# Performance work log

Measured on AMD Instinct MI355X. Metric: run time of the kernel, lower is better.

The kernel has to match this reference:

```python
import jax, jax.numpy as jnp
import numpy as np

H_DIM_EXP = 25  # n = 2**25 = 33,554,432

def setup_inputs() -> dict:
    key = jax.random.key(0)
    x = jax.random.normal(key, (2 ** H_DIM_EXP,), dtype=jnp.float32)
    return {"x": x, "h_dim_exp": H_DIM_EXP}

def reference(x, h_dim_exp):
    # Fast Walsh-Hadamard transform. The original views x as [1,2,2,...,2,1]
    # and applies a (+,-) butterfly along each of the log2(n) axes-of-size-2.
    # Butterfly stages on distinct bits commute, so we process bits from low
    # to high with rank-3 reshapes instead of a rank-(exp+2) tensor.
    y = x
    for i in range(h_dim_exp):
        y = y.reshape(-1, 2, 2 ** i)        # (n/2^{i+1}, 2, 2^i)
        a, b = y[:, 0, :], y[:, 1, :]
        y = jnp.stack([a + b, a - b], axis=1)
    return y.reshape(x.shape)
```

## Files before the change

kernel.cpp:

```cpp
#include <hip/hip_runtime.h>


__device__ __forceinline__ void bfly(float4& a, float4& b) {
  float ax = a.x, ay = a.y, az = a.z, aw = a.w;
  a.x = ax + b.x; a.y = ay + b.y; a.z = az + b.z; a.w = aw + b.w;
  b.x = ax - b.x; b.y = ay - b.y; b.z = az - b.z; b.w = aw - b.w;
}

__device__ __forceinline__ void cross4(float4 (&v)[16]) {
#pragma unroll
  for (int m = 0; m < 4; ++m) {
#pragma unroll
    for (int k = 0; k < 16; ++k) {
      if (!(k & (1 << m))) bfly(v[k], v[k | (1 << m)]);
    }
  }
}

__global__ __launch_bounds__(256) void wht_pass1(const float4* __restrict__ in4,
                                                 float4* __restrict__ out4) {
  __shared__ float4 lds[4096];
  const int t = threadIdx.x;
  const int base4 = (int)blockIdx.x << 12;
  float4 v[16];
#pragma unroll
  for (int k = 0; k < 16; ++k) v[k] = in4[base4 + t + (k << 8)];
#pragma unroll
  for (int k = 0; k < 16; ++k) {
    float4 a = v[k];
    float s0 = a.x + a.y, d0 = a.x - a.y, s1 = a.z + a.w, d1 = a.z - a.w;
    v[k].x = s0 + s1; v[k].y = d0 + d1; v[k].z = s0 - s1; v[k].w = d0 - d1;
  }
  cross4(v);

#pragma unroll
  for (int k = 0; k < 16; ++k) { int q = t + (k << 8); lds[q ^ ((q >> 4) & 15)] = v[k]; }
  __syncthreads();
#pragma unroll
  for (int u = 0; u < 16; ++u) { int q = u + (t << 4); v[u] = lds[q ^ ((q >> 4) & 15)]; }
  cross4(v);

#pragma unroll
  for (int u = 0; u < 16; ++u) { int q = u + (t << 4); lds[q ^ ((q >> 4) & 15)] = v[u]; }
  __syncthreads();
  const int c0 = t & 15, c1 = t >> 4;
#pragma unroll
  for (int u = 0; u < 16; ++u) {
    int q = c0 + (u << 4) + (c1 << 8);
    v[u] = lds[q ^ ((q >> 4) & 15)];
  }
  cross4(v);

#pragma unroll
  for (int u = 0; u < 16; ++u) out4[base4 + c0 + (u << 4) + (c1 << 8)] = v[u];
}

__global__ __launch_bounds__(1024, 4) void wht_pass2(float4* __restrict__ b4) {
  __shared__ float4 lds[4096];
  const int t = threadIdx.x;
  const int cb4 = (int)blockIdx.x << 3;
  const int c4 = t & 7;
  const int cc = t & 1;
  const int qt = (t >> 1) & 3;
  const int rlo = t >> 3;
  float4 v[16];
#pragma unroll
  for (int k = 0; k < 16; ++k)
    v[k] = b4[((long)(rlo + (k << 7)) << 12) + cb4 + c4];
  cross4(v);

#pragma unroll 1
  for (int r4 = 0; r4 < 4; ++r4) {
    __syncthreads();
    if (qt == r4) {
#pragma unroll
      for (int k = 0; k < 16; ++k) {
        int q = ((rlo + (k << 7)) << 1) | cc;
        lds[q ^ (((q >> 8) & 3) << 1)] = v[k];
      }
    }
    __syncthreads();
    if (qt == r4) {
#pragma unroll
      for (int rb = 0; rb < 16; ++rb) {
        int q = ((rb + (rlo << 4)) << 1) | cc;
        v[rb] = lds[q ^ (((q >> 8) & 3) << 1)];
      }
    }
  }
  cross4(v);

  const int rlowC = (t >> 3) & 15;
  const int rhi4C = (t & 1) | (((t >> 7) & 7) << 1);
#pragma unroll 1
  for (int r4 = 0; r4 < 4; ++r4) {
    __syncthreads();
    if (qt == r4) {
#pragma unroll
      for (int rb = 0; rb < 16; ++rb) {
        int q = ((rb + (rlo << 4)) << 1) | cc;
        lds[q ^ (((q >> 8) & 3) << 1)] = v[rb];
      }
    }
    __syncthreads();
    if (qt == r4) {
#pragma unroll
      for (int i = 0; i < 16; ++i) {
        int rm = i & 7, c = i >> 3;
        int r = rlowC + (rm << 4) + (rhi4C << 7);
        int q = (r << 1) | c;
        v[i] = lds[q ^ (((q >> 8) & 3) << 1)];
      }
    }
  }
#pragma unroll
  for (int m = 0; m < 3; ++m) {
#pragma unroll
    for (int i = 0; i < 16; ++i) {
      if (!(i & (1 << m))) bfly(v[i], v[i | (1 << m)]);
    }
  }

#pragma unroll
  for (int i = 0; i < 16; ++i) {
    int rm = i & 7, c = i >> 3;
    int r = rlowC + (rm << 4) + (rhi4C << 7);
    b4[((long)r << 12) + cb4 + (qt << 1) + c] = v[i];
  }
}

extern "C" void kernel_launch(void* const* d_in, const int* in_sizes, int n_in,
                              void* d_out, int out_size, void* d_ws, size_t ws_size,
                              hipStream_t stream) {
  (void)in_sizes; (void)n_in; (void)d_ws; (void)ws_size; (void)out_size;
  const float* x = (const float*)d_in[0];
  float* out = (float*)d_out;
  wht_pass1<<<2048, 256, 0, stream>>>((const float4*)x, (float4*)out);
  wht_pass2<<<512, 1024, 0, stream>>>((float4*)out);
}
```

Baseline: 306.8 us.

## Restructure WHT passes with half-size LDS staging and wave shuffles

```diff
diff --git a/kernel.cpp b/kernel.cpp
--- a/kernel.cpp
+++ b/kernel.cpp
@@ -9,20 +9,21 @@
 
 __device__ __forceinline__ void cross4(float4 (&v)[16]) {
 #pragma unroll
-  for (int m = 0; m < 4; ++m) {
+  for (int m = 0; m < 4; ++m)
 #pragma unroll
-    for (int k = 0; k < 16; ++k) {
+    for (int k = 0; k < 16; ++k)
       if (!(k & (1 << m))) bfly(v[k], v[k | (1 << m)]);
-    }
-  }
 }
 
-__global__ __launch_bounds__(256) void wht_pass1(const float4* __restrict__ in4,
-                                                 float4* __restrict__ out4) {
-  __shared__ float4 lds[4096];
+__device__ __forceinline__ int sw1(int q) { return q ^ (((q >> 4) ^ (q >> 3)) & 7); }
+
+__global__ __launch_bounds__(256, 4) void wht_pass1(const float4* __restrict__ in4,
+                                                    float4* __restrict__ out4) {
+  __shared__ float4 lds[2048];
   const int t = threadIdx.x;
   const int base4 = (int)blockIdx.x << 12;
-  float4 v[16];
+  const int t3 = (t >> 3) & 1, t54 = (t >> 4) & 3, t6 = (t >> 6) & 1, t7 = (t >> 7) & 1;
+  float4 v[16], u[16];
 #pragma unroll
   for (int k = 0; k < 16; ++k) v[k] = in4[base4 + t + (k << 8)];
 #pragma unroll
@@ -34,98 +35,104 @@
   cross4(v);
 
 #pragma unroll
-  for (int k = 0; k < 16; ++k) { int q = t + (k << 8); lds[q ^ ((q >> 4) & 15)] = v[k]; }
-  __syncthreads();
+  for (int j = 0; j < 2; ++j) {
+    __syncthreads();
 #pragma unroll
-  for (int u = 0; u < 16; ++u) { int q = u + (t << 4); v[u] = lds[q ^ ((q >> 4) & 15)]; }
+    for (int a = 0; a < 4; ++a)
+#pragma unroll
+      for (int b = 0; b < 2; ++b)
+        lds[sw1(t | (b << 8) | (a << 9))] = v[b | (j << 1) | (a << 2)];
+    __syncthreads();
+    if (t7 == j) {
+      const int rb = ((t & 7) << 4) | (t6 << 7) | (t3 << 8) | (t54 << 9);
+#pragma unroll
+      for (int k = 0; k < 16; ++k) u[k] = lds[sw1(rb | k)];
+    }
+  }
+  cross4(u);
+
+#pragma unroll
+  for (int j = 0; j < 2; ++j) {
+    __syncthreads();
+    {
+      const int wb = ((t & 7) << 3) | (t6 << 6) | (t3 << 7) | (t7 << 8) | (t54 << 9);
+#pragma unroll
+      for (int m = 0; m < 8; ++m) lds[sw1(wb | m)] = u[(j << 3) | m];
+    }
+    __syncthreads();
+    if (t6 == j) {
+      const int rb = (t & 7) | (t3 << 7) | (t7 << 8) | (t54 << 9);
+#pragma unroll
+      for (int k = 0; k < 16; ++k) v[k] = lds[sw1(rb | (k << 3))];
+    }
+  }
   cross4(v);
 
+  const int sb = (t & 7) | (t6 << 3) | (t3 << 8) | (t7 << 9) | (t54 << 10);
 #pragma unroll
-  for (int u = 0; u < 16; ++u) { int q = u + (t << 4); lds[q ^ ((q >> 4) & 15)] = v[u]; }
-  __syncthreads();
-  const int c0 = t & 15, c1 = t >> 4;
+  for (int k = 0; k < 16; ++k) out4[base4 + (sb | (k << 4))] = v[k];
+}
+
+__device__ __forceinline__ void shfl_bfly(float4 (&v)[16], const int mask) {
+  const float s = (threadIdx.x & mask) ? -1.f : 1.f;
 #pragma unroll
-  for (int u = 0; u < 16; ++u) {
-    int q = c0 + (u << 4) + (c1 << 8);
-    v[u] = lds[q ^ ((q >> 4) & 15)];
+  for (int k = 0; k < 16; ++k) {
+    float4 p;
+    p.x = __shfl_xor(v[k].x, mask, 64);
+    p.y = __shfl_xor(v[k].y, mask, 64);
+    p.z = __shfl_xor(v[k].z, mask, 64);
+    p.w = __shfl_xor(v[k].w, mask, 64);
+    v[k].x = fmaf(s, v[k].x, p.x);
+    v[k].y = fmaf(s, v[k].y, p.y);
+    v[k].z = fmaf(s, v[k].z, p.z);
+    v[k].w = fmaf(s, v[k].w, p.w);
+  }
+}
+
+__global__ __launch_bounds__(1024) void wht_pass2(float4* __restrict__ b4) {
+  __shared__ float4 lds[4096];
+  const int t = threadIdx.x;
+  const int cb4 = (int)blockIdx.x << 3;
+  const int c = t & 7, lam = (t >> 3) & 7, w = t >> 6;
+  float4 v[16];
+#pragma unroll
+  for (int k = 0; k < 16; ++k) {
+    const int r = w | (lam << 4) | (k << 7);
+    v[k] = b4[(r << 12) | cb4 | c];
+  }
+  cross4(v);
+  shfl_bfly(v, 8);
+  shfl_bfly(v, 16);
+  shfl_bfly(v, 32);
+
+  const int wq = w & 3;
+  const int ibase = c | (w << 3) | (lam << 7);
+  const int rbase = c | (lam << 7) | ((w >> 2) << 10);
+#pragma unroll
+  for (int j = 0; j < 4; ++j) {
+    const int q = j ^ wq;
+    __syncthreads();
+#pragma unroll
+    for (int Q = 0; Q < 4; ++Q)
+      if (q == Q) {
+#pragma unroll
+        for (int s = 0; s < 4; ++s) lds[ibase | (s << 10)] = v[Q | (s << 2)];
+      }
+    __syncthreads();
+#pragma unroll
+    for (int Q = 0; Q < 4; ++Q)
+      if (q == Q) {
+#pragma unroll
+        for (int s = 0; s < 4; ++s)
+          v[Q | (s << 2)] = lds[rbase | ((Q | (s << 2)) << 3)];
+      }
   }
   cross4(v);
 
 #pragma unroll
-  for (int u = 0; u < 16; ++u) out4[base4 + c0 + (u << 4) + (c1 << 8)] = v[u];
-}
-
-__global__ __launch_bounds__(1024, 4) void wht_pass2(float4* __restrict__ b4) {
-  __shared__ float4 lds[4096];
-  const int t = threadIdx.x;
-  const int cb4 = (int)blockIdx.x << 3;
-  const int c4 = t & 7;
-  const int cc = t & 1;
-  const int qt = (t >> 1) & 3;
-  const int rlo = t >> 3;
-  float4 v[16];
-#pragma unroll
-  for (int k = 0; k < 16; ++k)
-    v[k] = b4[((long)(rlo + (k << 7)) << 12) + cb4 + c4];
-  cross4(v);
-
-#pragma unroll 1
-  for (int r4 = 0; r4 < 4; ++r4) {
-    __syncthreads();
-    if (qt == r4) {
-#pragma unroll
-      for (int k = 0; k < 16; ++k) {
-        int q = ((rlo + (k << 7)) << 1) | cc;
-        lds[q ^ (((q >> 8) & 3) << 1)] = v[k];
-      }
-    }
-    __syncthreads();
-    if (qt == r4) {
-#pragma unroll
-      for (int rb = 0; rb < 16; ++rb) {
-        int q = ((rb + (rlo << 4)) << 1) | cc;
-        v[rb] = lds[q ^ (((q >> 8) & 3) << 1)];
-      }
-    }
-  }
-  cross4(v);
-
-  const int rlowC = (t >> 3) & 15;
-  const int rhi4C = (t & 1) | (((t >> 7) & 7) << 1);
-#pragma unroll 1
-  for (int r4 = 0; r4 < 4; ++r4) {
-    __syncthreads();
-    if (qt == r4) {
-#pragma unroll
-      for (int rb = 0; rb < 16; ++rb) {
-        int q = ((rb + (rlo << 4)) << 1) | cc;
-        lds[q ^ (((q >> 8) & 3) << 1)] = v[rb];
-      }
-    }
-    __syncthreads();
-    if (qt == r4) {
-#pragma unroll
-      for (int i = 0; i < 16; ++i) {
-        int rm = i & 7, c = i >> 3;
-        int r = rlowC + (rm << 4) + (rhi4C << 7);
-        int q = (r << 1) | c;
-        v[i] = lds[q ^ (((q >> 8) & 3) << 1)];
-      }
-    }
-  }
-#pragma unroll
-  for (int m = 0; m < 3; ++m) {
-#pragma unroll
-    for (int i = 0; i < 16; ++i) {
-      if (!(i & (1 << m))) bfly(v[i], v[i | (1 << m)]);
-    }
-  }
-
-#pragma unroll
-  for (int i = 0; i < 16; ++i) {
-    int rm = i & 7, c = i >> 3;
-    int r = rlowC + (rm << 4) + (rhi4C << 7);
-    b4[((long)r << 12) + cb4 + (qt << 1) + c] = v[i];
+  for (int k = 0; k < 16; ++k) {
+    const int r = k | (lam << 4) | (w << 7);
+    b4[(r << 12) | cb4 | c] = v[k];
   }
 }
 
```

Result: slower. 377.9 us (+23.2%).
